# Kernel tuning notes

Hardware: AMD Instinct MI355X
Metric: run time of the kernel (lower is better)

Reference implementation:

```python
import jax, jax.numpy as jnp
import numpy as np

EPS = 1e-5

def bn_relu(y, g, b):
    # BatchNorm1d in training mode: stats over (B, L) per channel, biased variance
    mu = jnp.mean(y, axis=(0, 2), keepdims=True)
    var = jnp.var(y, axis=(0, 2), keepdims=True)
    yn = (y - mu) * jax.lax.rsqrt(var + EPS)
    return jax.nn.relu(yn * g[None, :, None] + b[None, :, None])

def conv1x1_pad1(x, W):
    # Conv1d(k=1, padding=1, bias=False): pointwise matmul then zero-pad length by 1 each side
    y = jnp.einsum('bcl,oc->bol', x, W)
    return jnp.pad(y, ((0, 0), (0, 0), (1, 1)))

def conv1x1(x, W, b):
    return jnp.einsum('bcl,oc->bol', x, W) + b[None, :, None]

def conv3_pad1(x, W):
    # Conv1d(k=3, padding=1, bias=False); W: [O, C, 3]
    return jax.lax.conv_general_dilated(x, W, window_strides=(1,), padding=((1, 1),),
                                        dimension_numbers=('NCH', 'OIH', 'NCH'))

def pam(f, Wq, bq, Wk, bk, Wv, bv, gamma):
    q = conv1x1(f, Wq, bq)          # [B, C//8, L]
    k = conv1x1(f, Wk, bk)          # [B, C//8, L]
    v = conv1x1(f, Wv, bv)          # [B, C, L]
    energy = jnp.einsum('bql,bqm->blm', q, k)   # [B, L, L]
    attn = jax.nn.softmax(energy, axis=-1)
    out = jnp.einsum('bcm,blm->bcl', v, attn)
    return gamma * out + f

def cam(f, gamma):
    energy = jnp.einsum('bcl,bdl->bcd', f, f)    # [B, C, C]
    energy_new = jnp.max(energy, axis=-1, keepdims=True) - energy
    attn = jax.nn.softmax(energy_new, axis=-1)
    out = jnp.einsum('bcd,bdl->bcl', attn, f)
    return gamma * out + f

def setup_inputs() -> dict:
    key = jax.random.key(0)
    ks = jax.random.split(key, 24)
    B, C, L = 8, 256, 2046
    IC, OC = C // 4, 128  # inter_channels=64, out_channels
    s = 0.05
    d = {
        'x':   jax.random.normal(ks[0], (B, C, L), jnp.float32),
        'W5a': jax.random.normal(ks[1], (IC, C), jnp.float32) * s,
        'g5a': jnp.ones((IC,), jnp.float32), 'b5a': jnp.zeros((IC,), jnp.float32),
        'W5c': jax.random.normal(ks[2], (IC, C), jnp.float32) * s,
        'g5c': jnp.ones((IC,), jnp.float32), 'b5c': jnp.zeros((IC,), jnp.float32),
        'Wq':  jax.random.normal(ks[3], (IC // 8, IC), jnp.float32) * s,
        'bq':  jnp.zeros((IC // 8,), jnp.float32),
        'Wk':  jax.random.normal(ks[4], (IC // 8, IC), jnp.float32) * s,
        'bk':  jnp.zeros((IC // 8,), jnp.float32),
        'Wv':  jax.random.normal(ks[5], (IC, IC), jnp.float32) * s,
        'bv':  jnp.zeros((IC,), jnp.float32),
        'gamma_pam': jnp.full((1,), 0.1, jnp.float32),
        'gamma_cam': jnp.full((1,), 0.1, jnp.float32),
        'W51': jax.random.normal(ks[6], (IC, IC, 3), jnp.float32) * s,
        'g51': jnp.ones((IC,), jnp.float32), 'b51': jnp.zeros((IC,), jnp.float32),
        'W52': jax.random.normal(ks[7], (IC, IC, 3), jnp.float32) * s,
        'g52': jnp.ones((IC,), jnp.float32), 'b52': jnp.zeros((IC,), jnp.float32),
        'W6':  jax.random.normal(ks[8], (OC, IC), jnp.float32) * s,
        'b6':  jnp.zeros((OC,), jnp.float32),
        'W7':  jax.random.normal(ks[9], (OC, IC), jnp.float32) * s,
        'b7':  jnp.zeros((OC,), jnp.float32),
        'W8':  jax.random.normal(ks[10], (OC, IC), jnp.float32) * s,
        'b8':  jnp.zeros((OC,), jnp.float32),
    }
    return d

def reference(x, W5a, g5a, b5a, W5c, g5c, b5c, Wq, bq, Wk, bk, Wv, bv,
              gamma_pam, gamma_cam, W51, g51, b51, W52, g52, b52,
              W6, b6, W7, b7, W8, b8):
    # dropout (p=0.1) treated as identity (eval mode)
    feat1 = bn_relu(conv1x1_pad1(x, W5a), g5a, b5a)          # [B, IC, L+2]
    sa_feat = pam(feat1, Wq, bq, Wk, bk, Wv, bv, gamma_pam)
    sa_conv = bn_relu(conv3_pad1(sa_feat, W51), g51, b51)
    sa_output = conv1x1(sa_conv, W6, b6)                     # [B, OC, L+2]
    feat2 = bn_relu(conv1x1_pad1(x, W5c), g5c, b5c)
    sc_feat = cam(feat2, gamma_cam)
    sc_conv = bn_relu(conv3_pad1(sc_feat, W52), g52, b52)
    sc_output = conv1x1(sc_conv, W7, b7)
    feat_sum = sa_conv + sc_conv
    sasc = conv1x1(feat_sum, W8, b8)
    # pool == 'maxpool' selects AdaptiveAvgPool1d(1) in the original (note swap)
    sasc = jnp.mean(sasc, axis=-1)                            # [B, OC]
    return (sasc, sa_output, sc_output)
```

## Files before the change

### kernel.cpp

```cpp
#include <hip/hip_runtime.h>
#include <math.h>

#define B 8
#define C 256
#define L 2046
#define LP 2048
#define IC 64
#define OC 128
#define BN_EPS 1e-5f
#define INVN (1.f / 16384.f)

#define OFF_Y1T    0u
#define OFF_Y2C    524288u
#define OFF_Y51T   2097152u
#define OFF_Y52T   2621440u
#define OFF_VB     3145728u
#define OFF_QT     3670016u
#define OFF_KT     3735552u
#define OFF_EPART  3866624u
#define OFF_STATS1 4423680u
#define OFF_STATS2 4424704u
#define OFF_W5BF   4425728u
#define OFF_W67    4442112u
#define OFF_WT     4450304u
#define OFF_WQKV   4462592u
#define OFF_BQKV   4465152u

typedef __attribute__((ext_vector_type(8))) short bshort8;
typedef __attribute__((ext_vector_type(4))) float f32x4;

__device__ __forceinline__ unsigned short f2bf(float f) {
    union { float f; unsigned int u; } v; v.f = f;
    return (unsigned short)((v.u + 0x8000u) >> 16);
}
__device__ __forceinline__ float bf2f(unsigned short u) {
    union { unsigned int i; float f; } v; v.i = ((unsigned int)u) << 16;
    return v.f;
}
__device__ __forceinline__ unsigned int pk2(float a, float b) {
    union { float f; unsigned int u; } va, vb; va.f = a; vb.f = b;
    return __builtin_amdgcn_perm(vb.u + 0x8000u, va.u + 0x8000u, 0x07060302u);
}

__device__ __forceinline__ void load_coef(const float* __restrict__ STATS,
        const float* __restrict__ g, const float* __restrict__ beta,
        int base, int cnt, float* cA, float* cB) {
    int t = threadIdx.x;
    if (t < cnt) {
        int ch = base + t;
        float s = STATS[ch * 2] + STATS[256 + ch * 2] + STATS[512 + ch * 2] + STATS[768 + ch * 2];
        float q = STATS[ch * 2 + 1] + STATS[256 + ch * 2 + 1] + STATS[512 + ch * 2 + 1] + STATS[768 + ch * 2 + 1];
        float mu = s * INVN;
        float var = q * INVN - mu * mu;
        float A = g[t] * rsqrtf(var + BN_EPS);
        cA[t] = A;
        cB[t] = beta[t] - mu * A;
    }
}

__global__ __launch_bounds__(256) void k_wprep(
        const float* __restrict__ W5a, const float* __restrict__ W5c,
        const float* __restrict__ W6, const float* __restrict__ W7,
        const float* __restrict__ W51, const float* __restrict__ W52,
        const float* __restrict__ Wq, const float* __restrict__ Wk,
        const float* __restrict__ Wv, const float* __restrict__ bq,
        const float* __restrict__ bk, const float* __restrict__ bv,
        const float* __restrict__ b8,
        unsigned short* __restrict__ W5BF, unsigned short* __restrict__ W67,
        unsigned short* __restrict__ WT, unsigned short* __restrict__ WQKV,
        float* __restrict__ BQKV, float* __restrict__ STATS1,
        float* __restrict__ STATS2, float* __restrict__ out_sasc) {
    int i = blockIdx.x * 256 + threadIdx.x;
    if (i < 32768) {
        int o = i >> 8, c = i & 255;
        W5BF[i] = f2bf(o < 64 ? W5a[o * 256 + c] : W5c[(o - 64) * 256 + c]);
    } else if (i < 49152) {
        int j = i - 32768; int g = j >> 13; int r = j & 8191;
        W67[j] = f2bf(g ? W7[r] : W6[r]);
    } else if (i < 73728) {
        int j = i - 49152;
        int c = j & 63, o = (j >> 6) & 63, wt = j >> 12; int w = wt / 3, t = wt % 3;
        const float* Ws = w ? W52 : W51;
        WT[j] = f2bf(Ws[(o * 64 + c) * 3 + t]);
    } else if (i < 78848) {
        int j = i - 73728; int o = j >> 6, c = j & 63;
        float v = o < 8 ? Wq[o * 64 + c] : (o < 16 ? Wk[(o - 8) * 64 + c] : Wv[(o - 16) * 64 + c]);
        WQKV[j] = f2bf(v);
    } else if (i < 78928) {
        int o = i - 78848;
        BQKV[o] = o < 8 ? bq[o] : (o < 16 ? bk[o - 8] : bv[o - 16]);
    } else if (i < 80976) {
        int j = i - 78928;
        if (j < 1024) STATS1[j] = 0.f; else STATS2[j - 1024] = 0.f;
    } else if (i < 82000) {
        int j = i - 80976;
        out_sasc[j] = b8[j & 127];
    }
}

__global__ __launch_bounds__(256) void k_conv1(const float* __restrict__ x,
        const unsigned short* __restrict__ W5BF,
        unsigned short* __restrict__ Y1T, unsigned short* __restrict__ Y2C,
        float* __restrict__ STATS1) {
    __shared__ unsigned short xt[64][264];
    __shared__ float lds_part[4][64];
    int lt = blockIdx.x, b = blockIdx.y;
    int l0 = lt * 64;
    int t = threadIdx.x;
    {
        int j = t & 63, cg = t >> 6;
        int ls = l0 - 1 + j;
        bool ok = (ls >= 0) && (ls < L);
        const float* xs = x + (size_t)(b * C + cg * 64) * L + ls;
        unsigned short* row = &xt[j][cg * 64];
#pragma unroll
        for (int c8 = 0; c8 < 8; ++c8) {
            unsigned int pk[4];
#pragma unroll
            for (int i = 0; i < 4; ++i) {
                float v0 = ok ? xs[(size_t)(c8 * 8 + 2 * i) * L] : 0.f;
                float v1 = ok ? xs[(size_t)(c8 * 8 + 2 * i + 1) * L] : 0.f;
                pk[i] = pk2(v0, v1);
            }
            *(uint4*)(row + c8 * 8) = *(const uint4*)pk;
        }
    }
    __syncthreads();
    int w = t >> 6, lane = t & 63, n = lane & 15, quad = lane >> 4;
    bshort8 wf[2][8];
#pragma unroll
    for (int oi = 0; oi < 2; ++oi)
#pragma unroll
        for (int kt = 0; kt < 8; ++kt)
            wf[oi][kt] = *(const bshort8*)(W5BF + (size_t)((w * 2 + oi) * 16 + n) * C + kt * 32 + quad * 8);
    f32x4 acc[2][4];
#pragma unroll
    for (int oi = 0; oi < 2; ++oi)
#pragma unroll
        for (int sub = 0; sub < 4; ++sub) acc[oi][sub] = (f32x4){0.f, 0.f, 0.f, 0.f};
#pragma unroll
    for (int sub = 0; sub < 4; ++sub) {
        int lloc = sub * 16 + n;
#pragma unroll
        for (int kt = 0; kt < 8; ++kt) {
            bshort8 xb = *(const bshort8*)(&xt[lloc][kt * 32 + quad * 8]);
            acc[0][sub] = __builtin_amdgcn_mfma_f32_16x16x32_bf16(wf[0][kt], xb, acc[0][sub], 0, 0, 0);
            acc[1][sub] = __builtin_amdgcn_mfma_f32_16x16x32_bf16(wf[1][kt], xb, acc[1][sub], 0, 0, 0);
        }
    }
    if (w < 2) {
#pragma unroll
        for (int sub = 0; sub < 4; ++sub) {
            int lp = l0 + sub * 16 + n;
#pragma unroll
            for (int oi = 0; oi < 2; ++oi) {
                int ot = w * 2 + oi;
                uint2 pv;
                pv.x = pk2(acc[oi][sub][0], acc[oi][sub][1]);
                pv.y = pk2(acc[oi][sub][2], acc[oi][sub][3]);
                *(uint2*)(Y1T + ((size_t)(b * LP + lp)) * IC + ot * 16 + quad * 4) = pv;
            }
        }
    } else {
#pragma unroll
        for (int oi = 0; oi < 2; ++oi) {
            int ot = (w - 2) * 2 + oi;
#pragma unroll
            for (int r = 0; r < 4; ++r) {
                int o = ot * 16 + quad * 4 + r;
                unsigned short* dst = Y2C + ((size_t)(b * IC + o)) * LP + l0;
#pragma unroll
                for (int sub = 0; sub < 4; ++sub)
                    dst[sub * 16 + n] = f2bf(acc[oi][sub][r]);
            }
        }
    }
#pragma unroll
    for (int oi = 0; oi < 2; ++oi)
#pragma unroll
        for (int r = 0; r < 4; ++r) {
            float s = 0.f, q = 0.f;
#pragma unroll
            for (int sub = 0; sub < 4; ++sub) {
                float v = acc[oi][sub][r];
                s += v; q += v * v;
            }
#pragma unroll
            for (int msk = 1; msk < 16; msk <<= 1) {
                s += __shfl_xor(s, msk, 64);
                q += __shfl_xor(q, msk, 64);
            }
            if (n == 0) {
                int ci = oi * 16 + quad * 4 + r;
                lds_part[w][ci * 2] = s;
                lds_part[w][ci * 2 + 1] = q;
            }
        }
    __syncthreads();
    {
        int ch = t >> 1, wsrc = ch >> 5;
        int idx = ((ch & 31) << 1) | (t & 1);
        atomicAdd(&STATS1[(blockIdx.x & 3) * 256 + t], lds_part[wsrc][idx]);
    }
}

__device__ void role_qkv(char* dynsm, int lt, int b,
        const unsigned short* __restrict__ Y1T, const float* __restrict__ STATS1,
        const float* __restrict__ g5a, const float* __restrict__ b5a,
        const unsigned short* __restrict__ WQKV, const float* __restrict__ BQKV,
        unsigned short* __restrict__ QT, unsigned short* __restrict__ KT,
        unsigned short* __restrict__ VB) {
    float* cA = (float*)dynsm;
    float* cB = cA + 64;
    load_coef(STATS1, g5a, b5a, 0, 64, cA, cB);
    __syncthreads();
    int t = threadIdx.x;
    int w = t >> 6, lane = t & 63, n = lane & 15, quad = lane >> 4;
    int lrow = lt * 64 + w * 16 + n;
    bshort8 fb[2];
#pragma unroll
    for (int kt = 0; kt < 2; ++kt) {
        bshort8 raw = *(const bshort8*)(Y1T + ((size_t)(b * LP + lrow)) * IC + kt * 32 + quad * 8);
        bshort8 f;
#pragma unroll
        for (int j = 0; j < 8; ++j) {
            int c = kt * 32 + quad * 8 + j;
            float v = fmaxf(fmaf(cA[c], bf2f((unsigned short)raw[j]), cB[c]), 0.f);
            ((unsigned short*)&f)[j] = f2bf(v);
        }
        fb[kt] = f;
    }
    f32x4 acc[5];
#pragma unroll
    for (int ot = 0; ot < 5; ++ot) {
        f32x4 a = {0.f, 0.f, 0.f, 0.f};
#pragma unroll
        for (int kt = 0; kt < 2; ++kt) {
            bshort8 wf = *(const bshort8*)(WQKV + (size_t)(ot * 16 + n) * IC + kt * 32 + quad * 8);
            a = __builtin_amdgcn_mfma_f32_16x16x32_bf16(wf, fb[kt], a, 0, 0, 0);
        }
        acc[ot] = a;
    }
#pragma unroll
    for (int ot = 0; ot < 5; ++ot)
#pragma unroll
        for (int r = 0; r < 4; ++r) {
            int o = ot * 16 + quad * 4 + r;
            unsigned short bv16 = f2bf(acc[ot][r] + BQKV[o]);
            if (ot == 0) {
                if (o < 8) QT[((size_t)(b * LP + lrow)) * 8 + o] = bv16;
                else KT[((size_t)(b * LP + lrow)) * 8 + (o - 8)] = bv16;
            } else {
                VB[((size_t)(b * IC + (o - 16))) * LP + lrow] = bv16;
            }
        }
}

__device__ void role_gram(char* dynsm, int blk, int b,
        const unsigned short* __restrict__ Y2C, const float* __restrict__ STATS1,
        const float* __restrict__ g5c, const float* __restrict__ b5c,
        float* __restrict__ EPART) {
    float* cA = (float*)dynsm;
    float* cB = cA + 64;
    load_coef(STATS1, g5c, b5c, 64, 64, cA, cB);
    __syncthreads();
    int t = threadIdx.x;
    int w = t >> 6, lane = t & 63, n = lane & 15, quad = lane >> 4;
    f32x4 acc[4][4];
#pragma unroll
    for (int ti = 0; ti < 4; ++ti)
#pragma unroll
        for (int tj = 0; tj < 4; ++tj) acc[ti][tj] = (f32x4){0.f, 0.f, 0.f, 0.f};
    for (int chunk = 0; chunk < 4; ++chunk) {
        int lb = (blk * 4 + w) * 128 + chunk * 32 + quad * 8;
        bshort8 frag[4];
#pragma unroll
        for (int g = 0; g < 4; ++g) {
            int c = g * 16 + n;
            bshort8 raw = *(const bshort8*)(Y2C + ((size_t)(b * IC + c)) * LP + lb);
            bshort8 f;
            float A = cA[c], Bc = cB[c];
#pragma unroll
            for (int j = 0; j < 8; ++j)
                ((unsigned short*)&f)[j] = f2bf(fmaxf(fmaf(A, bf2f((unsigned short)raw[j]), Bc), 0.f));
            frag[g] = f;
        }
#pragma unroll
        for (int ti = 0; ti < 4; ++ti)
#pragma unroll
            for (int tj = 0; tj < 4; ++tj)
                acc[ti][tj] = __builtin_amdgcn_mfma_f32_16x16x32_bf16(frag[ti], frag[tj], acc[ti][tj], 0, 0, 0);
    }
    float* ep = EPART + ((size_t)(b * 16 + blk * 4 + w)) * 4096;
#pragma unroll
    for (int ti = 0; ti < 4; ++ti)
#pragma unroll
        for (int tj = 0; tj < 4; ++tj)
#pragma unroll
            for (int r = 0; r < 4; ++r)
                ep[(ti * 16 + quad * 4 + r) * 64 + tj * 16 + n] = acc[ti][tj][r];
}

__global__ __launch_bounds__(256) void k_fuse1(
        const unsigned short* __restrict__ Y1T, const unsigned short* __restrict__ Y2C,
        const float* __restrict__ STATS1,
        const float* __restrict__ g5a, const float* __restrict__ b5a,
        const float* __restrict__ g5c, const float* __restrict__ b5c,
        const unsigned short* __restrict__ WQKV, const float* __restrict__ BQKV,
        unsigned short* __restrict__ QT, unsigned short* __restrict__ KT,
        unsigned short* __restrict__ VB, float* __restrict__ EPART) {
    extern __shared__ char dynsm[];
    int idx = blockIdx.x;
    if (idx < 256) role_qkv(dynsm, idx & 31, idx >> 5, Y1T, STATS1, g5a, b5a,
                            WQKV, BQKV, QT, KT, VB);
    else { int g = idx - 256; role_gram(dynsm, g & 3, g >> 2, Y2C, STATS1, g5c, b5c, EPART); }
}

__device__ __forceinline__ void conv3_from_tile(const unsigned short* tile,
        const unsigned short* __restrict__ WT, unsigned short* __restrict__ dst,
        int b, int l0, float* lds_part, float* __restrict__ STATS2,
        int og, int blockx) {
    int t = threadIdx.x;
    int w = t >> 6, lane = t & 63, n = lane & 15, quad = lane >> 4;
    int lrow = l0 + w * 16 + n;
    f32x4 acc[4];
#pragma unroll
    for (int ot = 0; ot < 4; ++ot) acc[ot] = (f32x4){0.f, 0.f, 0.f, 0.f};
#pragma unroll
    for (int t3 = 0; t3 < 3; ++t3) {
        int trow = w * 16 + n + t3;
        bshort8 fb0 = *(const bshort8*)(tile + trow * 72 + quad * 8);
        bshort8 fb1 = *(const bshort8*)(tile + trow * 72 + 32 + quad * 8);
#pragma unroll
        for (int ot = 0; ot < 4; ++ot) {
            bshort8 w0 = *(const bshort8*)(WT + ((size_t)(t3 * 64 + ot * 16 + n)) * IC + quad * 8);
            bshort8 w1 = *(const bshort8*)(WT + ((size_t)(t3 * 64 + ot * 16 + n)) * IC + 32 + quad * 8);
            acc[ot] = __builtin_amdgcn_mfma_f32_16x16x32_bf16(w0, fb0, acc[ot], 0, 0, 0);
            acc[ot] = __builtin_amdgcn_mfma_f32_16x16x32_bf16(w1, fb1, acc[ot], 0, 0, 0);
        }
    }
#pragma unroll
    for (int ot = 0; ot < 4; ++ot) {
        uint2 pv;
        pv.x = pk2(acc[ot][0], acc[ot][1]);
        pv.y = pk2(acc[ot][2], acc[ot][3]);
        *(uint2*)(dst + ((size_t)(b * LP + lrow)) * IC + ot * 16 + quad * 4) = pv;
    }
#pragma unroll
    for (int ot = 0; ot < 4; ++ot)
#pragma unroll
        for (int r = 0; r < 4; ++r) {
            float s = acc[ot][r], q = s * s;
#pragma unroll
            for (int msk = 1; msk < 16; msk <<= 1) {
                s += __shfl_xor(s, msk, 64);
                q += __shfl_xor(q, msk, 64);
            }
            if (n == 0) {
                int cch = ot * 16 + quad * 4 + r;
                lds_part[w * 128 + cch * 2] = s;
                lds_part[w * 128 + cch * 2 + 1] = q;
            }
        }
    __syncthreads();
    if (t < 128) {
        float s = lds_part[t] + lds_part[128 + t] + lds_part[256 + t] + lds_part[384 + t];
        atomicAdd(&STATS2[(blockx & 3) * 256 + og * 128 + t], s);
    }
}

__device__ void role_pam_full(char* dynsm, int qt, int b,
        const unsigned short* __restrict__ qT, const unsigned short* __restrict__ kT,
        const unsigned short* __restrict__ vb,
        const unsigned short* __restrict__ Y1T, const float* __restrict__ STATS1,
        const float* __restrict__ g5a, const float* __restrict__ b5a,
        const float* __restrict__ gamma, const unsigned short* __restrict__ WT,
        unsigned short* __restrict__ Y51T, float* __restrict__ STATS2) {
    float* os = (float*)dynsm;
    unsigned short* ps = (unsigned short*)(dynsm + 16640);
    unsigned short* tile = ps;
    float* cA = (float*)(dynsm + 25856);
    float* cB = cA + 64;
    float* dn = cB + 64;
    float* lds_part = dn + 64;
    int base = qt * 62 - 1;
    int tid = threadIdx.x;
    int wq = tid >> 6, lane = tid & 63, n = lane & 15, quad = lane >> 4;
    load_coef(STATS1, g5a, b5a, 0, 64, cA, cB);
    int qrow = base + wq * 16 + n;
    int qcl = qrow < 0 ? 0 : (qrow > LP - 1 ? LP - 1 : qrow);
    bshort8 qa = {};
    if (quad == 0)
        qa = *(const bshort8*)(qT + ((size_t)(b * LP + qcl)) * 8);
    f32x4 acc[4];
#pragma unroll
    for (int s = 0; s < 4; ++s) acc[s] = (f32x4){0.f, 0.f, 0.f, 0.f};
    float li[4] = {0.f, 0.f, 0.f, 0.f};
    unsigned short* pw = ps + wq * 16 * 72;

    bshort8 kb[4];
#pragma unroll
    for (int s = 0; s < 4; ++s) kb[s] = (bshort8){};
    if (quad == 0) {
#pragma unroll
        for (int s = 0; s < 4; ++s)
            kb[s] = *(const bshort8*)(kT + ((size_t)(b * LP + s * 16 + n)) * 8);
    }
    for (int it = 0; it < 32; ++it) {
        int m0 = it * 64;
        bshort8 vr[8];
#pragma unroll
        for (int step = 0; step < 2; ++step)
#pragma unroll
            for (int s = 0; s < 4; ++s)
                vr[step * 4 + s] = *(const bshort8*)(vb +
                    ((size_t)(b * IC + s * 16 + n)) * LP + m0 + step * 32 + quad * 8);
        bshort8 kn[4];
#pragma unroll
        for (int s = 0; s < 4; ++s) kn[s] = (bshort8){};
        if (it < 31 && quad == 0) {
            int m1 = m0 + 64;
#pragma unroll
            for (int s = 0; s < 4; ++s)
                kn[s] = *(const bshort8*)(kT + ((size_t)(b * LP + m1 + s * 16 + n)) * 8);
        }
        f32x4 sc[4];
#pragma unroll
        for (int s = 0; s < 4; ++s)
            sc[s] = __builtin_amdgcn_mfma_f32_16x16x32_bf16(qa, kb[s],
                        (f32x4){0.f, 0.f, 0.f, 0.f}, 0, 0, 0);
#pragma unroll
        for (int s = 0; s < 4; ++s)
#pragma unroll
            for (int r = 0; r < 4; ++r) {
                float p = __expf(sc[s][r]);
                li[r] += p;
                pw[(quad * 4 + r) * 72 + s * 16 + n] = f2bf(p);
            }
#pragma unroll
        for (int step = 0; step < 2; ++step) {
            bshort8 pa = *(const bshort8*)(pw + n * 72 + step * 32 + quad * 8);
#pragma unroll
            for (int s = 0; s < 4; ++s)
                acc[s] = __builtin_amdgcn_mfma_f32_16x16x32_bf16(pa, vr[step * 4 + s], acc[s], 0, 0, 0);
        }
#pragma unroll
        for (int s = 0; s < 4; ++s) kb[s] = kn[s];
    }
#pragma unroll
    for (int s = 0; s < 4; ++s)
#pragma unroll
        for (int r = 0; r < 4; ++r)
            os[(s * 16 + n) * 65 + wq * 16 + quad * 4 + r] = acc[s][r];
#pragma unroll
    for (int r = 0; r < 4; ++r) {
        float s_ = li[r];
#pragma unroll
        for (int msk = 1; msk < 16; msk <<= 1) s_ += __shfl_xor(s_, msk, 64);
        if (n == 0) dn[wq * 16 + quad * 4 + r] = s_;
    }
    __syncthreads();
    float gm = gamma[0];
    {
        int c = tid >> 2, qc = tid & 3;
#pragma unroll
        for (int i = 0; i < 16; ++i) {
            int r = qc * 16 + i;
            int absr = base + r;
            float val = 0.f;
            if (absr >= 0 && absr < LP) {
                unsigned short raw = Y1T[((size_t)(b * LP + absr)) * IC + c];
                float f1v = fmaxf(fmaf(cA[c], bf2f(raw), cB[c]), 0.f);
                val = fmaf(gm, os[c * 65 + r] / dn[r], f1v);
            }
            tile[r * 72 + c] = f2bf(val);
        }
    }
    __syncthreads();
    {
        int j = wq * 16 + n;
        int absout = base + 1 + j;
        bool valid = (j < 62) && (absout < LP);
        f32x4 a3[4];
#pragma unroll
        for (int ot = 0; ot < 4; ++ot) a3[ot] = (f32x4){0.f, 0.f, 0.f, 0.f};
#pragma unroll
        for (int t3 = 0; t3 < 3; ++t3) {
            bshort8 fb0 = *(const bshort8*)(tile + (j + t3) * 72 + quad * 8);
            bshort8 fb1 = *(const bshort8*)(tile + (j + t3) * 72 + 32 + quad * 8);
#pragma unroll
            for (int ot = 0; ot < 4; ++ot) {
                bshort8 w0 = *(const bshort8*)(WT + ((size_t)(t3 * 64 + ot * 16 + n)) * IC + quad * 8);
                bshort8 w1 = *(const bshort8*)(WT + ((size_t)(t3 * 64 + ot * 16 + n)) * IC + 32 + quad * 8);
                a3[ot] = __builtin_amdgcn_mfma_f32_16x16x32_bf16(w0, fb0, a3[ot], 0, 0, 0);
                a3[ot] = __builtin_amdgcn_mfma_f32_16x16x32_bf16(w1, fb1, a3[ot], 0, 0, 0);
            }
        }
        if (valid) {
#pragma unroll
            for (int ot = 0; ot < 4; ++ot) {
                uint2 pv;
                pv.x = pk2(a3[ot][0], a3[ot][1]);
                pv.y = pk2(a3[ot][2], a3[ot][3]);
                *(uint2*)(Y51T + ((size_t)(b * LP + absout)) * IC + ot * 16 + quad * 4) = pv;
            }
        }
#pragma unroll
        for (int ot = 0; ot < 4; ++ot)
#pragma unroll
            for (int r = 0; r < 4; ++r) {
                float s = valid ? a3[ot][r] : 0.f;
                float q = s * s;
#pragma unroll
                for (int msk = 1; msk < 16; msk <<= 1) {
                    s += __shfl_xor(s, msk, 64);
                    q += __shfl_xor(q, msk, 64);
                }
                if (n == 0) {
                    int cch = ot * 16 + quad * 4 + r;
                    lds_part[wq * 128 + cch * 2] = s;
                    lds_part[wq * 128 + cch * 2 + 1] = q;
                }
            }
        __syncthreads();
        if (tid < 128) {
            float s = lds_part[tid] + lds_part[128 + tid] + lds_part[256 + tid] + lds_part[384 + tid];
            atomicAdd(&STATS2[(qt & 3) * 256 + tid], s);
        }
    }
}

__device__ void role_cam_full(char* dynsm, int lt, int b,
        const float* __restrict__ EPART, const unsigned short* __restrict__ Y2C,
        const float* __restrict__ STATS1,
        const float* __restrict__ g5c, const float* __restrict__ b5c,
        const float* __restrict__ gamma, const unsigned short* __restrict__ WT,
        unsigned short* __restrict__ Y52T, float* __restrict__ STATS2) {
    float* as = (float*)dynsm;
    float* cA = as + 4096; float* cB = cA + 64;
    unsigned short* tile = (unsigned short*)(cB + 64);
    float* lds_part = (float*)(tile + 4752);
    int l0 = lt * 64;
    int t = threadIdx.x;
    load_coef(STATS1, g5c, b5c, 64, 64, cA, cB);
    for (int idx = t; idx < 4096; idx += 256) {
        float s = 0.f;
#pragma unroll
        for (int ch = 0; ch < 16; ++ch) s += EPART[((size_t)(b * 16 + ch)) * 4096 + idx];
        as[idx] = s;
    }
    __syncthreads();
    {
        int row = t >> 2, qd = t & 3;
        float v[16];
#pragma unroll
        for (int i = 0; i < 16; ++i) v[i] = as[row * 64 + qd * 16 + i];
        float mn = v[0];
#pragma unroll
        for (int i = 1; i < 16; ++i) mn = fminf(mn, v[i]);
        mn = fminf(mn, __shfl_xor(mn, 1, 64));
        mn = fminf(mn, __shfl_xor(mn, 2, 64));
        float s = 0.f;
#pragma unroll
        for (int i = 0; i < 16; ++i) { v[i] = __expf(mn - v[i]); s += v[i]; }
        s += __shfl_xor(s, 1, 64);
        s += __shfl_xor(s, 2, 64);
        float inv = 1.f / s;
#pragma unroll
        for (int i = 0; i < 16; ++i) as[row * 64 + qd * 16 + i] = v[i] * inv;
    }
    __syncthreads();
    float gm = gamma[0];
    {
        int lq = t & 63, cg = t >> 6;
        const unsigned short* fb = Y2C + (size_t)b * IC * LP + l0 + lq;
        float acc[16];
#pragma unroll
        for (int i = 0; i < 16; ++i) acc[i] = 0.f;
        for (int d4 = 0; d4 < 16; ++d4) {
            float fv[4];
#pragma unroll
            for (int i = 0; i < 4; ++i) {
                int d = 4 * d4 + i;
                fv[i] = fmaxf(fmaf(cA[d], bf2f(fb[(size_t)d * LP]), cB[d]), 0.f);
            }
#pragma unroll
            for (int cc = 0; cc < 16; ++cc) {
                const float4 a4 = *reinterpret_cast<const float4*>(as + (cg * 16 + cc) * 64 + d4 * 4);
                acc[cc] += a4.x * fv[0] + a4.y * fv[1] + a4.z * fv[2] + a4.w * fv[3];
            }
        }
#pragma unroll
        for (int cc = 0; cc < 16; ++cc) {
            int c = cg * 16 + cc;
            float res = fmaxf(fmaf(cA[c], bf2f(fb[(size_t)c * LP]), cB[c]), 0.f);
            tile[(1 + lq) * 72 + c] = f2bf(fmaf(gm, acc[cc], res));
        }
    }
    float* fcol = lds_part;
    if (t < 128) {
        int row = t >> 6;
        int ch = t & 63;
        int l = l0 - 1 + row * 65;
        float v = 0.f;
        if (l >= 0 && l < LP)
            v = fmaxf(fmaf(cA[ch], bf2f(Y2C[(size_t)b * IC * LP + (size_t)ch * LP + l]), cB[ch]), 0.f);
        fcol[row * 64 + ch] = v;
    }
    __syncthreads();
    if (t < 128) {
        int sel = t & 1;
        int row = sel ? 65 : 0;
        int ch = t >> 1;
        int l = l0 - 1 + (sel ? 65 : 0);
        float val = 0.f;
        if (l >= 0 && l < LP) {
            const float* fc = fcol + sel * 64;
            float a = 0.f;
#pragma unroll 8
            for (int d = 0; d < 64; ++d) a = fmaf(as[ch * 64 + d], fc[d], a);
            val = fmaf(gm, a, fc[ch]);
        }
        tile[row * 72 + ch] = f2bf(val);
    }
    __syncthreads();
    conv3_from_tile(tile, WT, Y52T, b, l0, lds_part, STATS2, 1, lt);
}

__global__ __launch_bounds__(256) void k_fuse2(
        const unsigned short* __restrict__ QT, const unsigned short* __restrict__ KT,
        const unsigned short* __restrict__ VB,
        const unsigned short* __restrict__ Y1T, const unsigned short* __restrict__ Y2C,
        const float* __restrict__ STATS1,
        const float* __restrict__ g5a, const float* __restrict__ b5a,
        const float* __restrict__ g5c, const float* __restrict__ b5c,
        const float* __restrict__ gpam, const float* __restrict__ gcam,
        const float* __restrict__ EPART, const unsigned short* __restrict__ WTall,
        unsigned short* __restrict__ Y51T, unsigned short* __restrict__ Y52T,
        float* __restrict__ STATS2) {
    extern __shared__ char dynsm[];
    int idx = blockIdx.x;
    if (idx < 272) {
        int b = idx / 34; int qt = idx - b * 34;
        role_pam_full(dynsm, qt, b, QT, KT, VB, Y1T, STATS1, g5a, b5a, gpam,
                      WTall, Y51T, STATS2);
    } else {
        int g = idx - 272;
        role_cam_full(dynsm, g & 31, g >> 5, EPART, Y2C, STATS1, g5c, b5c, gcam,
                      WTall + 12288, Y52T, STATS2);
    }
}

__global__ __launch_bounds__(256) void k_final(const unsigned short* __restrict__ Y51T,
        const unsigned short* __restrict__ Y52T, const float* __restrict__ STATS2,
        const float* __restrict__ g51, const float* __restrict__ b51,
        const float* __restrict__ g52, const float* __restrict__ b52,
        const unsigned short* __restrict__ W67,
        const float* __restrict__ b6, const float* __restrict__ b7,
        const float* __restrict__ W8,
        float* __restrict__ out_sa, float* __restrict__ out_sc,
        float* __restrict__ out_sasc) {
    __shared__ float cA[128], cB[128];
    __shared__ float fsw[4][64];
    __shared__ float chsum[64];
    int lt = blockIdx.x, og = blockIdx.y, b = blockIdx.z;
    int t = threadIdx.x;
    if (t < 128) {
        float s = STATS2[t * 2] + STATS2[256 + t * 2] + STATS2[512 + t * 2] + STATS2[768 + t * 2];
        float q = STATS2[t * 2 + 1] + STATS2[256 + t * 2 + 1] + STATS2[512 + t * 2 + 1] + STATS2[768 + t * 2 + 1];
        float mu = s * INVN, var = q * INVN - mu * mu;
        float gv = t < 64 ? g51[t] : g52[t - 64];
        float bv = t < 64 ? b51[t] : b52[t - 64];
        float A = gv * rsqrtf(var + BN_EPS);
        cA[t] = A; cB[t] = bv - mu * A;
    }
    __syncthreads();
    int w = t >> 6, lane = t & 63, n = lane & 15, quad = lane >> 4;
    int lrow = lt * 64 + w * 16 + n;
    float fs_lane[16];
    bshort8 ba[2], bb[2];
#pragma unroll
    for (int kt = 0; kt < 2; ++kt) {
        bshort8 ra = *(const bshort8*)(Y51T + ((size_t)(b * LP + lrow)) * IC + kt * 32 + quad * 8);
        bshort8 rb = *(const bshort8*)(Y52T + ((size_t)(b * LP + lrow)) * IC + kt * 32 + quad * 8);
        bshort8 fa, fb;
#pragma unroll
        for (int j = 0; j < 8; ++j) {
            int c = kt * 32 + quad * 8 + j;
            float v1 = fmaxf(fmaf(cA[c], bf2f((unsigned short)ra[j]), cB[c]), 0.f);
            float v2 = fmaxf(fmaf(cA[64 + c], bf2f((unsigned short)rb[j]), cB[64 + c]), 0.f);
            ((unsigned short*)&fa)[j] = f2bf(v1);
            ((unsigned short*)&fb)[j] = f2bf(v2);
            fs_lane[kt * 8 + j] = v1 + v2;
        }
        ba[kt] = fa; bb[kt] = fb;
    }
    f32x4 accA[4], accB[4];
#pragma unroll
    for (int ot = 0; ot < 4; ++ot) {
        accA[ot] = (f32x4){0.f, 0.f, 0.f, 0.f};
        accB[ot] = (f32x4){0.f, 0.f, 0.f, 0.f};
    }
#pragma unroll
    for (int ot = 0; ot < 4; ++ot)
#pragma unroll
        for (int kt = 0; kt < 2; ++kt) {
            bshort8 wa = *(const bshort8*)(W67 + (size_t)(og * 64 + ot * 16 + n) * IC + kt * 32 + quad * 8);
            bshort8 wb = *(const bshort8*)(W67 + 8192 + (size_t)(og * 64 + ot * 16 + n) * IC + kt * 32 + quad * 8);
            accA[ot] = __builtin_amdgcn_mfma_f32_16x16x32_bf16(wa, ba[kt], accA[ot], 0, 0, 0);
            accB[ot] = __builtin_amdgcn_mfma_f32_16x16x32_bf16(wb, bb[kt], accB[ot], 0, 0, 0);
        }
#pragma unroll
    for (int ot = 0; ot < 4; ++ot)
#pragma unroll
        for (int r = 0; r < 4; ++r) {
            int o = og * 64 + ot * 16 + quad * 4 + r;
            out_sa[((size_t)(b * OC + o)) * LP + lrow] = accA[ot][r] + b6[o];
            out_sc[((size_t)(b * OC + o)) * LP + lrow] = accB[ot][r] + b7[o];
        }
    if (og == 0) {
#pragma unroll
        for (int i = 0; i < 16; ++i) {
            float s = fs_lane[i];
#pragma unroll
            for (int msk = 1; msk < 16; msk <<= 1) s += __shfl_xor(s, msk, 64);
            if (n == 0) {
                int c = (i >> 3) * 32 + quad * 8 + (i & 7);
                fsw[w][c] = s;
            }
        }
        __syncthreads();
        if (t < 64) chsum[t] = fsw[0][t] + fsw[1][t] + fsw[2][t] + fsw[3][t];
        __syncthreads();
        if (t < 128) {
            float s = 0.f;
            for (int c = 0; c < 64; ++c) s = fmaf(W8[t * 64 + c], chsum[c], s);
            atomicAdd(&out_sasc[b * OC + t], s * (1.f / (float)LP));
        }
    }
}

extern "C" void kernel_launch(void* const* d_in, const int* in_sizes, int n_in,
                              void* d_out, int out_size, void* d_ws, size_t ws_size,
                              hipStream_t stream) {
    (void)in_sizes; (void)n_in; (void)out_size; (void)ws_size;
    const float* x    = (const float*)d_in[0];
    const float* W5a  = (const float*)d_in[1];
    const float* g5a  = (const float*)d_in[2];
    const float* b5a  = (const float*)d_in[3];
    const float* W5c  = (const float*)d_in[4];
    const float* g5c  = (const float*)d_in[5];
    const float* b5c  = (const float*)d_in[6];
    const float* Wq   = (const float*)d_in[7];
    const float* bq   = (const float*)d_in[8];
    const float* Wk   = (const float*)d_in[9];
    const float* bk   = (const float*)d_in[10];
    const float* Wv   = (const float*)d_in[11];
    const float* bv   = (const float*)d_in[12];
    const float* gpam = (const float*)d_in[13];
    const float* gcam = (const float*)d_in[14];
    const float* W51  = (const float*)d_in[15];
    const float* g51  = (const float*)d_in[16];
    const float* b51  = (const float*)d_in[17];
    const float* W52  = (const float*)d_in[18];
    const float* g52  = (const float*)d_in[19];
    const float* b52  = (const float*)d_in[20];
    const float* W6   = (const float*)d_in[21];
    const float* b6   = (const float*)d_in[22];
    const float* W7   = (const float*)d_in[23];
    const float* b7   = (const float*)d_in[24];
    const float* W8   = (const float*)d_in[25];
    const float* b8   = (const float*)d_in[26];

    float* ws = (float*)d_ws;
    float* out = (float*)d_out;
    unsigned short* Y1T  = (unsigned short*)(ws + OFF_Y1T);
    unsigned short* Y2C  = (unsigned short*)(ws + OFF_Y2C);
    unsigned short* Y51T = (unsigned short*)(ws + OFF_Y51T);
    unsigned short* Y52T = (unsigned short*)(ws + OFF_Y52T);
    unsigned short* VB   = (unsigned short*)(ws + OFF_VB);
    unsigned short* QT   = (unsigned short*)(ws + OFF_QT);
    unsigned short* KT   = (unsigned short*)(ws + OFF_KT);
    float* EPART  = ws + OFF_EPART;
    float* STATS1 = ws + OFF_STATS1;
    float* STATS2 = ws + OFF_STATS2;
    unsigned short* W5BF = (unsigned short*)(ws + OFF_W5BF);
    unsigned short* W67  = (unsigned short*)(ws + OFF_W67);
    unsigned short* WT   = (unsigned short*)(ws + OFF_WT);
    unsigned short* WQKV = (unsigned short*)(ws + OFF_WQKV);
    float* BQKV = ws + OFF_BQKV;

    float* out_sa = out + B * OC;
    float* out_sc = out + B * OC + (size_t)B * OC * LP;

    k_wprep<<<321, 256, 0, stream>>>(W5a, W5c, W6, W7, W51, W52, Wq, Wk, Wv,
                                     bq, bk, bv, b8, W5BF, W67, WT, WQKV, BQKV,
                                     STATS1, STATS2, out);
    k_conv1<<<dim3(32, B), 256, 0, stream>>>(x, W5BF, Y1T, Y2C, STATS1);
    k_fuse1<<<288, 256, 512, stream>>>(Y1T, Y2C, STATS1, g5a, b5a, g5c, b5c,
                                       WQKV, BQKV, QT, KT, VB, EPART);
    k_fuse2<<<528, 256, 28672, stream>>>(QT, KT, VB, Y1T, Y2C, STATS1,
                                         g5a, b5a, g5c, b5c, gpam, gcam,
                                         EPART, WT, Y51T, Y52T, STATS2);
    k_final<<<dim3(32, 2, B), 256, 0, stream>>>(Y51T, Y52T, STATS2, g51, b51, g52, b52,
                                                W67, b6, b7, W8, out_sa, out_sc, out);
}
```

Baseline: 250.6 us.

## Use 512-thread blocks in fuse2: split PAM keys across waves, pack two CAM tiles

The fused attention kernel now launches 512-thread blocks. PAM blocks split the key range into two halves handled by separate wave groups, then merge the partial numerators and denominators through LDS before the conv3 stage. The conv3 output channels are also divided across the wave groups. CAM blocks pack two independent 256-thread tiles per block, each with its own LDS region. This halves the serial key loop per PAM block and raises parallelism, at the cost of doubling LDS per block, which may reduce occupancy, and adding an extra reduction pass.

```diff
diff --git a/kernel.cpp b/kernel.cpp
--- a/kernel.cpp
+++ b/kernel.cpp
@@ -44,8 +44,7 @@
 
 __device__ __forceinline__ void load_coef(const float* __restrict__ STATS,
         const float* __restrict__ g, const float* __restrict__ beta,
-        int base, int cnt, float* cA, float* cB) {
-    int t = threadIdx.x;
+        int base, int cnt, float* cA, float* cB, int t) {
     if (t < cnt) {
         int ch = base + t;
         float s = STATS[ch * 2] + STATS[256 + ch * 2] + STATS[512 + ch * 2] + STATS[768 + ch * 2];
@@ -212,7 +211,7 @@
         unsigned short* __restrict__ VB) {
     float* cA = (float*)dynsm;
     float* cB = cA + 64;
-    load_coef(STATS1, g5a, b5a, 0, 64, cA, cB);
+    load_coef(STATS1, g5a, b5a, 0, 64, cA, cB, threadIdx.x);
     __syncthreads();
     int t = threadIdx.x;
     int w = t >> 6, lane = t & 63, n = lane & 15, quad = lane >> 4;
@@ -262,7 +261,7 @@
         float* __restrict__ EPART) {
     float* cA = (float*)dynsm;
     float* cB = cA + 64;
-    load_coef(STATS1, g5c, b5c, 64, 64, cA, cB);
+    load_coef(STATS1, g5c, b5c, 64, 64, cA, cB, threadIdx.x);
     __syncthreads();
     int t = threadIdx.x;
     int w = t >> 6, lane = t & 63, n = lane & 15, quad = lane >> 4;
@@ -316,58 +315,8 @@
     else { int g = idx - 256; role_gram(dynsm, g & 3, g >> 2, Y2C, STATS1, g5c, b5c, EPART); }
 }
 
-__device__ __forceinline__ void conv3_from_tile(const unsigned short* tile,
-        const unsigned short* __restrict__ WT, unsigned short* __restrict__ dst,
-        int b, int l0, float* lds_part, float* __restrict__ STATS2,
-        int og, int blockx) {
-    int t = threadIdx.x;
-    int w = t >> 6, lane = t & 63, n = lane & 15, quad = lane >> 4;
-    int lrow = l0 + w * 16 + n;
-    f32x4 acc[4];
-#pragma unroll
-    for (int ot = 0; ot < 4; ++ot) acc[ot] = (f32x4){0.f, 0.f, 0.f, 0.f};
-#pragma unroll
-    for (int t3 = 0; t3 < 3; ++t3) {
-        int trow = w * 16 + n + t3;
-        bshort8 fb0 = *(const bshort8*)(tile + trow * 72 + quad * 8);
-        bshort8 fb1 = *(const bshort8*)(tile + trow * 72 + 32 + quad * 8);
-#pragma unroll
-        for (int ot = 0; ot < 4; ++ot) {
-            bshort8 w0 = *(const bshort8*)(WT + ((size_t)(t3 * 64 + ot * 16 + n)) * IC + quad * 8);
-            bshort8 w1 = *(const bshort8*)(WT + ((size_t)(t3 * 64 + ot * 16 + n)) * IC + 32 + quad * 8);
-            acc[ot] = __builtin_amdgcn_mfma_f32_16x16x32_bf16(w0, fb0, acc[ot], 0, 0, 0);
-            acc[ot] = __builtin_amdgcn_mfma_f32_16x16x32_bf16(w1, fb1, acc[ot], 0, 0, 0);
-        }
-    }
-#pragma unroll
-    for (int ot = 0; ot < 4; ++ot) {
-        uint2 pv;
-        pv.x = pk2(acc[ot][0], acc[ot][1]);
-        pv.y = pk2(acc[ot][2], acc[ot][3]);
-        *(uint2*)(dst + ((size_t)(b * LP + lrow)) * IC + ot * 16 + quad * 4) = pv;
-    }
-#pragma unroll
-    for (int ot = 0; ot < 4; ++ot)
-#pragma unroll
-        for (int r = 0; r < 4; ++r) {
-            float s = acc[ot][r], q = s * s;
-#pragma unroll
-            for (int msk = 1; msk < 16; msk <<= 1) {
-                s += __shfl_xor(s, msk, 64);
-                q += __shfl_xor(q, msk, 64);
-            }
-            if (n == 0) {
-                int cch = ot * 16 + quad * 4 + r;
-                lds_part[w * 128 + cch * 2] = s;
-                lds_part[w * 128 + cch * 2 + 1] = q;
-            }
-        }
-    __syncthreads();
-    if (t < 128) {
-        float s = lds_part[t] + lds_part[128 + t] + lds_part[256 + t] + lds_part[384 + t];
-        atomicAdd(&STATS2[(blockx & 3) * 256 + og * 128 + t], s);
-    }
-}
+
+#define CAM_HALF_BYTES 28448
 
 __device__ void role_pam_full(char* dynsm, int qt, int b,
         const unsigned short* __restrict__ qT, const unsigned short* __restrict__ kT,
@@ -377,17 +326,19 @@
         const float* __restrict__ gamma, const unsigned short* __restrict__ WT,
         unsigned short* __restrict__ Y51T, float* __restrict__ STATS2) {
     float* os = (float*)dynsm;
-    unsigned short* ps = (unsigned short*)(dynsm + 16640);
+    unsigned short* ps = (unsigned short*)(dynsm + 33280);
     unsigned short* tile = ps;
-    float* cA = (float*)(dynsm + 25856);
+    float* cA = (float*)(dynsm + 51712);
     float* cB = cA + 64;
     float* dn = cB + 64;
-    float* lds_part = dn + 64;
+    float* lds_part = dn + 128;
     int base = qt * 62 - 1;
     int tid = threadIdx.x;
-    int wq = tid >> 6, lane = tid & 63, n = lane & 15, quad = lane >> 4;
-    load_coef(STATS1, g5a, b5a, 0, 64, cA, cB);
-    int qrow = base + wq * 16 + n;
+    int w8 = tid >> 6;
+    int qsub = w8 & 3, kh = w8 >> 2;
+    int lane = tid & 63, n = lane & 15, quad = lane >> 4;
+    load_coef(STATS1, g5a, b5a, 0, 64, cA, cB, tid);
+    int qrow = base + qsub * 16 + n;
     int qcl = qrow < 0 ? 0 : (qrow > LP - 1 ? LP - 1 : qrow);
     bshort8 qa = {};
     if (quad == 0)
@@ -396,7 +347,8 @@
 #pragma unroll
     for (int s = 0; s < 4; ++s) acc[s] = (f32x4){0.f, 0.f, 0.f, 0.f};
     float li[4] = {0.f, 0.f, 0.f, 0.f};
-    unsigned short* pw = ps + wq * 16 * 72;
+    unsigned short* pw = ps + w8 * 16 * 72;
+    int mbase = kh * 1024;
 
     bshort8 kb[4];
 #pragma unroll
@@ -404,10 +356,10 @@
     if (quad == 0) {
 #pragma unroll
         for (int s = 0; s < 4; ++s)
-            kb[s] = *(const bshort8*)(kT + ((size_t)(b * LP + s * 16 + n)) * 8);
-    }
-    for (int it = 0; it < 32; ++it) {
-        int m0 = it * 64;
+            kb[s] = *(const bshort8*)(kT + ((size_t)(b * LP + mbase + s * 16 + n)) * 8);
+    }
+    for (int it = 0; it < 16; ++it) {
+        int m0 = mbase + it * 64;
         bshort8 vr[8];
 #pragma unroll
         for (int step = 0; step < 2; ++step)
@@ -418,7 +370,7 @@
         bshort8 kn[4];
 #pragma unroll
         for (int s = 0; s < 4; ++s) kn[s] = (bshort8){};
-        if (it < 31 && quad == 0) {
+        if (it < 15 && quad == 0) {
             int m1 = m0 + 64;
 #pragma unroll
             for (int s = 0; s < 4; ++s)
@@ -451,65 +403,70 @@
     for (int s = 0; s < 4; ++s)
 #pragma unroll
         for (int r = 0; r < 4; ++r)
-            os[(s * 16 + n) * 65 + wq * 16 + quad * 4 + r] = acc[s][r];
+            os[kh * 4160 + (s * 16 + n) * 65 + qsub * 16 + quad * 4 + r] = acc[s][r];
 #pragma unroll
     for (int r = 0; r < 4; ++r) {
         float s_ = li[r];
 #pragma unroll
         for (int msk = 1; msk < 16; msk <<= 1) s_ += __shfl_xor(s_, msk, 64);
-        if (n == 0) dn[wq * 16 + quad * 4 + r] = s_;
+        if (n == 0) dn[kh * 64 + qsub * 16 + quad * 4 + r] = s_;
     }
     __syncthreads();
     float gm = gamma[0];
     {
-        int c = tid >> 2, qc = tid & 3;
-#pragma unroll
-        for (int i = 0; i < 16; ++i) {
-            int r = qc * 16 + i;
+        int c = tid >> 3, qc = tid & 7;
+#pragma unroll
+        for (int i = 0; i < 8; ++i) {
+            int r = qc * 8 + i;
             int absr = base + r;
             float val = 0.f;
             if (absr >= 0 && absr < LP) {
                 unsigned short raw = Y1T[((size_t)(b * LP + absr)) * IC + c];
                 float f1v = fmaxf(fmaf(cA[c], bf2f(raw), cB[c]), 0.f);
-                val = fmaf(gm, os[c * 65 + r] / dn[r], f1v);
+                float o = os[c * 65 + r] + os[4160 + c * 65 + r];
+                float d = dn[r] + dn[64 + r];
+                val = fmaf(gm, o / d, f1v);
             }
             tile[r * 72 + c] = f2bf(val);
         }
     }
     __syncthreads();
     {
-        int j = wq * 16 + n;
+        int wp = w8 & 3, og2 = w8 >> 2;
+        int j = wp * 16 + n;
         int absout = base + 1 + j;
         bool valid = (j < 62) && (absout < LP);
-        f32x4 a3[4];
-#pragma unroll
-        for (int ot = 0; ot < 4; ++ot) a3[ot] = (f32x4){0.f, 0.f, 0.f, 0.f};
+        f32x4 a3[2];
+#pragma unroll
+        for (int oi = 0; oi < 2; ++oi) a3[oi] = (f32x4){0.f, 0.f, 0.f, 0.f};
 #pragma unroll
         for (int t3 = 0; t3 < 3; ++t3) {
             bshort8 fb0 = *(const bshort8*)(tile + (j + t3) * 72 + quad * 8);
             bshort8 fb1 = *(const bshort8*)(tile + (j + t3) * 72 + 32 + quad * 8);
 #pragma unroll
-            for (int ot = 0; ot < 4; ++ot) {
+            for (int oi = 0; oi < 2; ++oi) {
+                int ot = og2 * 2 + oi;
                 bshort8 w0 = *(const bshort8*)(WT + ((size_t)(t3 * 64 + ot * 16 + n)) * IC + quad * 8);
                 bshort8 w1 = *(const bshort8*)(WT + ((size_t)(t3 * 64 + ot * 16 + n)) * IC + 32 + quad * 8);
-                a3[ot] = __builtin_amdgcn_mfma_f32_16x16x32_bf16(w0, fb0, a3[ot], 0, 0, 0);
-                a3[ot] = __builtin_amdgcn_mfma_f32_16x16x32_bf16(w1, fb1, a3[ot], 0, 0, 0);
+                a3[oi] = __builtin_amdgcn_mfma_f32_16x16x32_bf16(w0, fb0, a3[oi], 0, 0, 0);
+                a3[oi] = __builtin_amdgcn_mfma_f32_16x16x32_bf16(w1, fb1, a3[oi], 0, 0, 0);
             }
         }
         if (valid) {
 #pragma unroll
-            for (int ot = 0; ot < 4; ++ot) {
+            for (int oi = 0; oi < 2; ++oi) {
+                int ot = og2 * 2 + oi;
                 uint2 pv;
-                pv.x = pk2(a3[ot][0], a3[ot][1]);
-                pv.y = pk2(a3[ot][2], a3[ot][3]);
+                pv.x = pk2(a3[oi][0], a3[oi][1]);
+                pv.y = pk2(a3[oi][2], a3[oi][3]);
                 *(uint2*)(Y51T + ((size_t)(b * LP + absout)) * IC + ot * 16 + quad * 4) = pv;
             }
         }
 #pragma unroll
-        for (int ot = 0; ot < 4; ++ot)
+        for (int oi = 0; oi < 2; ++oi)
 #pragma unroll
             for (int r = 0; r < 4; ++r) {
-                float s = valid ? a3[ot][r] : 0.f;
+                float s = valid ? a3[oi][r] : 0.f;
                 float q = s * s;
 #pragma unroll
                 for (int msk = 1; msk < 16; msk <<= 1) {
@@ -517,9 +474,9 @@
                     q += __shfl_xor(q, msk, 64);
                 }
                 if (n == 0) {
-                    int cch = ot * 16 + quad * 4 + r;
-                    lds_part[wq * 128 + cch * 2] = s;
-                    lds_part[wq * 128 + cch * 2 + 1] = q;
+                    int cch = (og2 * 2 + oi) * 16 + quad * 4 + r;
+                    lds_part[wp * 128 + cch * 2] = s;
+                    lds_part[wp * 128 + cch * 2 + 1] = q;
                 }
             }
         __syncthreads();
@@ -530,20 +487,71 @@
     }
 }
 
-__device__ void role_cam_full(char* dynsm, int lt, int b,
+__device__ __forceinline__ void conv3_from_tile_cam(const unsigned short* tile,
+        const unsigned short* __restrict__ WT, unsigned short* __restrict__ dst,
+        int b, int l0, float* lds_part, float* __restrict__ STATS2,
+        int blockx, int tl) {
+    int w = tl >> 6, lane = tl & 63, n = lane & 15, quad = lane >> 4;
+    int lrow = l0 + w * 16 + n;
+    f32x4 acc[4];
+#pragma unroll
+    for (int ot = 0; ot < 4; ++ot) acc[ot] = (f32x4){0.f, 0.f, 0.f, 0.f};
+#pragma unroll
+    for (int t3 = 0; t3 < 3; ++t3) {
+        int trow = w * 16 + n + t3;
+        bshort8 fb0 = *(const bshort8*)(tile + trow * 72 + quad * 8);
+        bshort8 fb1 = *(const bshort8*)(tile + trow * 72 + 32 + quad * 8);
+#pragma unroll
+        for (int ot = 0; ot < 4; ++ot) {
+            bshort8 w0 = *(const bshort8*)(WT + ((size_t)(t3 * 64 + ot * 16 + n)) * IC + quad * 8);
+            bshort8 w1 = *(const bshort8*)(WT + ((size_t)(t3 * 64 + ot * 16 + n)) * IC + 32 + quad * 8);
+            acc[ot] = __builtin_amdgcn_mfma_f32_16x16x32_bf16(w0, fb0, acc[ot], 0, 0, 0);
+            acc[ot] = __builtin_amdgcn_mfma_f32_16x16x32_bf16(w1, fb1, acc[ot], 0, 0, 0);
+        }
+    }
+#pragma unroll
+    for (int ot = 0; ot < 4; ++ot) {
+        uint2 pv;
+        pv.x = pk2(acc[ot][0], acc[ot][1]);
+        pv.y = pk2(acc[ot][2], acc[ot][3]);
+        *(uint2*)(dst + ((size_t)(b * LP + lrow)) * IC + ot * 16 + quad * 4) = pv;
+    }
+#pragma unroll
+    for (int ot = 0; ot < 4; ++ot)
+#pragma unroll
+        for (int r = 0; r < 4; ++r) {
+            float s = acc[ot][r], q = s * s;
+#pragma unroll
+            for (int msk = 1; msk < 16; msk <<= 1) {
+                s += __shfl_xor(s, msk, 64);
+                q += __shfl_xor(q, msk, 64);
+            }
+            if (n == 0) {
+                int cch = ot * 16 + quad * 4 + r;
+                lds_part[w * 128 + cch * 2] = s;
+                lds_part[w * 128 + cch * 2 + 1] = q;
+            }
+        }
+    __syncthreads();
+    if (tl < 128) {
+        float s = lds_part[tl] + lds_part[128 + tl] + lds_part[256 + tl] + lds_part[384 + tl];
+        atomicAdd(&STATS2[(blockx & 3) * 256 + 128 + tl], s);
+    }
+}
+
+__device__ void role_cam_full(char* sm, int tl, int lt, int b,
         const float* __restrict__ EPART, const unsigned short* __restrict__ Y2C,
         const float* __restrict__ STATS1,
         const float* __restrict__ g5c, const float* __restrict__ b5c,
         const float* __restrict__ gamma, const unsigned short* __restrict__ WT,
         unsigned short* __restrict__ Y52T, float* __restrict__ STATS2) {
-    float* as = (float*)dynsm;
+    float* as = (float*)sm;
     float* cA = as + 4096; float* cB = cA + 64;
     unsigned short* tile = (unsigned short*)(cB + 64);
     float* lds_part = (float*)(tile + 4752);
     int l0 = lt * 64;
-    int t = threadIdx.x;
-    load_coef(STATS1, g5c, b5c, 64, 64, cA, cB);
-    for (int idx = t; idx < 4096; idx += 256) {
+    load_coef(STATS1, g5c, b5c, 64, 64, cA, cB, tl);
+    for (int idx = tl; idx < 4096; idx += 256) {
         float s = 0.f;
 #pragma unroll
         for (int ch = 0; ch < 16; ++ch) s += EPART[((size_t)(b * 16 + ch)) * 4096 + idx];
@@ -551,7 +559,7 @@
     }
     __syncthreads();
     {
-        int row = t >> 2, qd = t & 3;
+        int row = tl >> 2, qd = tl & 3;
         float v[16];
 #pragma unroll
         for (int i = 0; i < 16; ++i) v[i] = as[row * 64 + qd * 16 + i];
@@ -572,7 +580,7 @@
     __syncthreads();
     float gm = gamma[0];
     {
-        int lq = t & 63, cg = t >> 6;
+        int lq = tl & 63, cg = tl >> 6;
         const unsigned short* fb = Y2C + (size_t)b * IC * LP + l0 + lq;
         float acc[16];
 #pragma unroll
@@ -598,9 +606,9 @@
         }
     }
     float* fcol = lds_part;
-    if (t < 128) {
-        int row = t >> 6;
-        int ch = t & 63;
+    if (tl < 128) {
+        int row = tl >> 6;
+        int ch = tl & 63;
         int l = l0 - 1 + row * 65;
         float v = 0.f;
         if (l >= 0 && l < LP)
@@ -608,10 +616,10 @@
         fcol[row * 64 + ch] = v;
     }
     __syncthreads();
-    if (t < 128) {
-        int sel = t & 1;
+    if (tl < 128) {
+        int sel = tl & 1;
         int row = sel ? 65 : 0;
-        int ch = t >> 1;
+        int ch = tl >> 1;
         int l = l0 - 1 + (sel ? 65 : 0);
         float val = 0.f;
         if (l >= 0 && l < LP) {
@@ -624,10 +632,10 @@
         tile[row * 72 + ch] = f2bf(val);
     }
     __syncthreads();
-    conv3_from_tile(tile, WT, Y52T, b, l0, lds_part, STATS2, 1, lt);
-}
-
-__global__ __launch_bounds__(256) void k_fuse2(
+    conv3_from_tile_cam(tile, WT, Y52T, b, l0, lds_part, STATS2, lt, tl);
+}
+
+__global__ __launch_bounds__(512) void k_fuse2(
         const unsigned short* __restrict__ QT, const unsigned short* __restrict__ KT,
         const unsigned short* __restrict__ VB,
         const unsigned short* __restrict__ Y1T, const unsigned short* __restrict__ Y2C,
@@ -646,7 +654,10 @@
                       WTall, Y51T, STATS2);
     } else {
         int g = idx - 272;
-        role_cam_full(dynsm, g & 31, g >> 5, EPART, Y2C, STATS1, g5c, b5c, gcam,
+        int half = threadIdx.x >> 8;
+        int j = g * 2 + half;
+        role_cam_full(dynsm + half * CAM_HALF_BYTES, threadIdx.x & 255,
+                      j & 31, j >> 5, EPART, Y2C, STATS1, g5c, b5c, gcam,
                       WTall + 12288, Y52T, STATS2);
     }
 }
@@ -799,7 +810,7 @@
     k_conv1<<<dim3(32, B), 256, 0, stream>>>(x, W5BF, Y1T, Y2C, STATS1);
     k_fuse1<<<288, 256, 512, stream>>>(Y1T, Y2C, STATS1, g5a, b5a, g5c, b5c,
                                        WQKV, BQKV, QT, KT, VB, EPART);
-    k_fuse2<<<528, 256, 28672, stream>>>(QT, KT, VB, Y1T, Y2C, STATS1,
+    k_fuse2<<<400, 512, 56896, stream>>>(QT, KT, VB, Y1T, Y2C, STATS1,
                                          g5a, b5a, g5c, b5c, gpam, gcam,
                                          EPART, WT, Y51T, Y52T, STATS2);
     k_final<<<dim3(32, 2, B), 256, 0, stream>>>(Y51T, Y52T, STATS2, g51, b51, g52, b52,
```

New measurement: 247.7 us. Within noise of the previous version (-1.2%).
